# Kernel tuning notes

Measured on AMD Instinct MI355X. Metric: run time of the kernel, lower is better.

## Reference

```python
import jax, jax.numpy as jnp
import numpy as np

B, S, L, H, C = 16, 2048, 256, 768, 512

def setup_inputs() -> dict:
    key = jax.random.key(0)
    ks = jax.random.split(key, 9)
    sc = 1.0 / np.sqrt(H)
    return {
        "input_hidden_states": jax.random.normal(ks[0], (B, S, H), jnp.float32),
        "label_hidden_states": jax.random.normal(ks[1], (L, H), jnp.float32),
        "Wi": jax.random.normal(ks[2], (C, H), jnp.float32) * sc,
        "bi": jnp.zeros((C,), jnp.float32),
        "Wl": jax.random.normal(ks[3], (C, H), jnp.float32) * sc,
        "bl": jnp.zeros((C,), jnp.float32),
        "Wia": jax.random.normal(ks[4], (C, H), jnp.float32) * sc,
        "bia": jnp.zeros((C,), jnp.float32),
        "Wla": jax.random.normal(ks[5], (C, H), jnp.float32) * sc,
        "bla": jnp.zeros((C,), jnp.float32),
        "context": jax.random.uniform(ks[6], (C,), jnp.float32),
        "Wp": jax.random.normal(ks[7], (H, C), jnp.float32) * (1.0 / np.sqrt(C)),
    }

def reference(input_hidden_states, label_hidden_states, Wi, bi, Wl, bl,
              Wia, bia, Wla, bla, context, Wp):
    # Dropout is identity in eval mode.
    x = input_hidden_states            # [B,S,H]
    lab = label_hidden_states          # [L,H] (original repeats over batch; math is identical)
    input_trans = jax.nn.sigmoid(jnp.einsum('bsh,ch->bsc', x, Wi) + bi)      # [B,S,C]
    label_trans = jax.nn.sigmoid(lab @ Wl.T + bl)                            # [L,C]
    input_attn = jax.nn.sigmoid(jnp.einsum('bsh,ch->bsc', x, Wia) + bia)    # [B,S,C]
    label_attn = jax.nn.sigmoid(lab @ Wla.T + bla)                          # [L,C]
    # attn logits: (context * input_attn) @ label_attn^T  -> [B,S,L]
    logits = jnp.einsum('bsc,lc->bsl', input_attn * context, label_attn)
    attn = jax.nn.softmax(logits, axis=-1)                                   # [B,S,L]
    # trilinear reduction: sum_{s,l} input_trans[b,s,c] * attn[b,s,l] * label_trans[l,c]
    weighted = jnp.einsum('bsl,lc->bsc', attn, label_trans)                  # [B,S,C]
    fusion = jnp.sum(input_trans * weighted, axis=1)                         # [B,C]
    return fusion @ Wp.T                                                     # [B,H]
```

## Files before the change

kernel.cpp:

```cpp
#include <hip/hip_runtime.h>

#define H_DIM 768
#define C_DIM 512
#define L_DIM 256
#define S_DIM 2048
#define B_DIM 16

#define IA_STRIDE 520
#define ATTN_STRIDE 264
#define XP_STRIDE 776

typedef __attribute__((ext_vector_type(8))) short short8;
typedef __attribute__((ext_vector_type(4))) float f32x4;
typedef __attribute__((ext_vector_type(2))) __fp16 half2v;

#define MFMA_F16(a, b, c) __builtin_amdgcn_mfma_f32_16x16x32_f16((a), (b), (c), 0, 0, 0)

__device__ __forceinline__ unsigned short f2h(float f) {
    _Float16 h = (_Float16)f;
    return __builtin_bit_cast(unsigned short, h);
}
__device__ __forceinline__ float h2f(unsigned short u) {
    _Float16 h = __builtin_bit_cast(_Float16, u);
    return (float)h;
}
__device__ __forceinline__ float sigmoid_f(float x) { return 1.0f / (1.0f + __expf(-x)); }

__device__ __forceinline__ short8 cvt8(const float* p) {
    const float4* q = (const float4*)(const void*)p;
    float4 u = q[0], v = q[1];
    half2v h0 = __builtin_amdgcn_cvt_pkrtz(u.x, u.y);
    half2v h1 = __builtin_amdgcn_cvt_pkrtz(u.z, u.w);
    half2v h2 = __builtin_amdgcn_cvt_pkrtz(v.x, v.y);
    half2v h3 = __builtin_amdgcn_cvt_pkrtz(v.z, v.w);
    int4 pk = { __builtin_bit_cast(int, h0), __builtin_bit_cast(int, h1),
                __builtin_bit_cast(int, h2), __builtin_bit_cast(int, h3) };
    return __builtin_bit_cast(short8, pk);
}


__global__ __launch_bounds__(256) void prep_w(
    const float* __restrict__ Wi, const float* __restrict__ Wia,
    const float* __restrict__ Wl, const float* __restrict__ Wla,
    unsigned short* __restrict__ Wi_f, unsigned short* __restrict__ Wia_f,
    unsigned short* __restrict__ Wl_f, unsigned short* __restrict__ Wla_f)
{
    const int tid = blockIdx.x * 256 + threadIdx.x;
    const int m   = tid / 49152;
    const int idx = tid - m * 49152;
    const int ct   = idx / 1536;
    const int rem  = idx - ct * 1536;
    const int kt   = rem >> 6;
    const int lane = rem & 63;
    const int row  = ct * 16 + (lane & 15);
    const int kcol = kt * 32 + (lane >> 4) * 8;
    const float* src = (m == 0 ? Wi : (m == 1 ? Wia : (m == 2 ? Wl : Wla)));
    unsigned short* dst = (m == 0 ? Wi_f : (m == 1 ? Wia_f : (m == 2 ? Wl_f : Wla_f)));
    short8 v = cvt8(src + (size_t)row * H_DIM + kcol);
    const int frag = ((ct >> 3) * 24 + kt) * 8 + (ct & 7);
    *(short8*)(void*)(dst + ((size_t)frag * 64 + lane) * 8) = v;
}

__global__ __launch_bounds__(256) void prep_x(
    const float* __restrict__ x, unsigned short* __restrict__ x_f)
{
    __shared__ unsigned short tile[16 * XP_STRIDE];
    const int t  = threadIdx.x;
    const int mt = blockIdx.x;
    const float4* src = (const float4*)(const void*)(x + (size_t)mt * 16 * H_DIM);
#pragma unroll
    for (int i = 0; i < 12; ++i) {
        const int id  = i * 256 + t;
        const int row = id / 192;
        const int c4  = id - row * 192;
        float4 v = src[id];
        half2v h0 = __builtin_amdgcn_cvt_pkrtz(v.x, v.y);
        half2v h1 = __builtin_amdgcn_cvt_pkrtz(v.z, v.w);
        uint2 pk = { __builtin_bit_cast(unsigned int, h0),
                     __builtin_bit_cast(unsigned int, h1) };
        *(uint2*)(void*)(tile + row * XP_STRIDE + c4 * 4) = pk;
    }
    __syncthreads();
    const int lane = t & 63;
    const int wave = t >> 6;
#pragma unroll
    for (int q = 0; q < 6; ++q) {
        const int kt = wave * 6 + q;
        short8 v = *(const short8*)(const void*)(
            tile + (lane & 15) * XP_STRIDE + kt * 32 + (lane >> 4) * 8);
        *(short8*)(void*)(x_f + ((size_t)(mt * 24 + kt) * 64 + lane) * 8) = v;
    }
}

__global__ __launch_bounds__(256) void label_mfma(
    const float* __restrict__ lab,
    const unsigned short* __restrict__ Wl_f,  const float* __restrict__ bl,
    const unsigned short* __restrict__ Wla_f, const float* __restrict__ bla,
    const float* __restrict__ ctx,
    unsigned short* __restrict__ la_f,
    unsigned short* __restrict__ lt_f)
{
    const int tid  = threadIdx.x;
    const int wave = tid >> 6;
    const int lane = tid & 63;
    const int quad = lane >> 4;
    const int c16  = lane & 15;
    const int ct2  = blockIdx.x & 7;
    const int mh   = blockIdx.x >> 3;
    const int ct   = ct2 * 4 + wave;
    const int n0   = ct * 16;
    const int l0   = mh * 32;

    const f32x4 z4 = {0.f, 0.f, 0.f, 0.f};
    f32x4 a1[2], a2[2];
#pragma unroll
    for (int mt = 0; mt < 2; ++mt) { a1[mt] = z4; a2[mt] = z4; }

    const float* lb = lab + (size_t)(l0 + c16) * H_DIM + quad * 8;
    const short8* wl8  = (const short8*)(const void*)Wl_f  + ((size_t)(ct >> 3) * 24 * 8 + (ct & 7)) * 64 + lane;
    const short8* wla8 = (const short8*)(const void*)Wla_f + ((size_t)(ct >> 3) * 24 * 8 + (ct & 7)) * 64 + lane;
    for (int kt = 0; kt < 24; ++kt) {
        short8 b1 = wl8[kt * 8 * 64];
        short8 b2 = wla8[kt * 8 * 64];
#pragma unroll
        for (int mt = 0; mt < 2; ++mt) {
            short8 a = cvt8(lb + mt * 16 * H_DIM + kt * 32);
            a1[mt] = MFMA_F16(a, b1, a1[mt]);
            a2[mt] = MFMA_F16(a, b2, a2[mt]);
        }
    }
    const int c = n0 + c16;
    const float blv = bl[c], blav = bla[c], cv = ctx[c];
#pragma unroll
    for (int mt = 0; mt < 2; ++mt)
#pragma unroll
        for (int r = 0; r < 4; ++r) {
            const int l = l0 + mt * 16 + quad * 4 + r;
            const float ltv = sigmoid_f(a1[mt][r] + blv);
            const float lav = sigmoid_f(a2[mt][r] + blav) * cv;
            {
                const int ctc = c >> 4, ktl = l >> 5;
                const int frag = ((ctc >> 3) * 8 + ktl) * 8 + (ctc & 7);
                const int ln = (c & 15) | (((l >> 3) & 3) << 4);
                lt_f[((size_t)frag * 64 + ln) * 8 + (l & 7)] = f2h(ltv);
            }
            {
                const int lt = l >> 4, ktc = c >> 5;
                const int frag = ((lt >> 2) * 16 + ktc) * 4 + (lt & 3);
                const int ln = (l & 15) | (((c >> 3) & 3) << 4);
                la_f[((size_t)frag * 64 + ln) * 8 + (c & 7)] = f2h(lav);
            }
        }
}

template<bool XF>
__global__ __launch_bounds__(512, 4) void fused_main(
    const unsigned short* __restrict__ x_f,
    const float* __restrict__ x,
    const float* __restrict__ bi,
    const float* __restrict__ bia,
    const unsigned short* __restrict__ Wi_f,
    const unsigned short* __restrict__ Wia_f,
    const unsigned short* __restrict__ lt_f,
    const unsigned short* __restrict__ la_f,
    float* __restrict__ fusion)
{
    __shared__ unsigned short lds_buf[64 * IA_STRIDE];
    __shared__ float rowscratch[8 * 64];
    __shared__ float inv_lds[64];

    const int tid  = threadIdx.x;
    const int wave = tid >> 6;
    const int lane = tid & 63;
    const int quad = lane >> 4;
    const int c16  = lane & 15;

    const int row0 = blockIdx.x * 64;
    const int b    = row0 >> 11;

    const f32x4 z4 = {0.f, 0.f, 0.f, 0.f};
    const int n0 = wave * 64;

    const float*  xb  = x + (size_t)(row0 + c16) * H_DIM + quad * 8;
    const short8* xf8 = (const short8*)(const void*)x_f + (size_t)blockIdx.x * 96 * 64 + lane;
    const size_t wofs = ((size_t)(wave >> 1) * 192 + (size_t)(wave & 1) * 4) * 64 + lane;

    {
        f32x4 acc[4][4];
#pragma unroll
        for (int m = 0; m < 4; ++m)
#pragma unroll
            for (int nt = 0; nt < 4; ++nt) acc[m][nt] = z4;
        const short8* wa8 = (const short8*)(const void*)Wia_f + wofs;
        for (int kt = 0; kt < 24; ++kt) {
            short8 a0, a1, a2, a3;
            if constexpr (XF) {
                a0 = xf8[kt * 64];        a1 = xf8[(24 + kt) * 64];
                a2 = xf8[(48 + kt) * 64]; a3 = xf8[(72 + kt) * 64];
            } else {
                a0 = cvt8(xb + kt * 32);                a1 = cvt8(xb + 16 * H_DIM + kt * 32);
                a2 = cvt8(xb + 32 * H_DIM + kt * 32);   a3 = cvt8(xb + 48 * H_DIM + kt * 32);
            }
#pragma unroll
            for (int nt = 0; nt < 4; ++nt) {
                short8 bw = wa8[(kt * 8 + nt) * 64];
                acc[0][nt] = MFMA_F16(a0, bw, acc[0][nt]);
                acc[1][nt] = MFMA_F16(a1, bw, acc[1][nt]);
                acc[2][nt] = MFMA_F16(a2, bw, acc[2][nt]);
                acc[3][nt] = MFMA_F16(a3, bw, acc[3][nt]);
            }
        }
#pragma unroll
        for (int nt = 0; nt < 4; ++nt) {
            const int col = n0 + nt * 16 + c16;
            const float bv = bia[col];
#pragma unroll
            for (int m = 0; m < 4; ++m)
#pragma unroll
                for (int r = 0; r < 4; ++r) {
                    const int row = m * 16 + quad * 4 + r;
                    lds_buf[row * IA_STRIDE + col] = f2h(sigmoid_f(acc[m][nt][r] + bv));
                }
        }
    }
    __syncthreads();

    const int n0l = wave * 32;
    f32x4 accl[4][2];
#pragma unroll
    for (int m = 0; m < 4; ++m)
#pragma unroll
        for (int j = 0; j < 2; ++j) accl[m][j] = z4;
    {
        const unsigned short* ab = lds_buf + c16 * IA_STRIDE + quad * 8;
        const short8* la8 = (const short8*)(const void*)la_f
                          + ((size_t)(wave >> 1) * 64 + (size_t)(wave & 1) * 2) * 64 + lane;
        for (int kt = 0; kt < 16; ++kt) {
            const int kk = kt * 32;
            short8 a0 = *(const short8*)(const void*)(ab + kk);
            short8 a1 = *(const short8*)(const void*)(ab + 16 * IA_STRIDE + kk);
            short8 a2 = *(const short8*)(const void*)(ab + 32 * IA_STRIDE + kk);
            short8 a3 = *(const short8*)(const void*)(ab + 48 * IA_STRIDE + kk);
#pragma unroll
            for (int j = 0; j < 2; ++j) {
                short8 bfr = la8[(kt * 4 + j) * 64];
                accl[0][j] = MFMA_F16(a0, bfr, accl[0][j]);
                accl[1][j] = MFMA_F16(a1, bfr, accl[1][j]);
                accl[2][j] = MFMA_F16(a2, bfr, accl[2][j]);
                accl[3][j] = MFMA_F16(a3, bfr, accl[3][j]);
            }
        }
    }
    __syncthreads();

    float rmax[4][4];
#pragma unroll
    for (int m = 0; m < 4; ++m)
#pragma unroll
        for (int r = 0; r < 4; ++r) {
            float mx = fmaxf(accl[m][0][r], accl[m][1][r]);
#pragma unroll
            for (int off = 1; off < 16; off <<= 1) mx = fmaxf(mx, __shfl_xor(mx, off, 64));
            rmax[m][r] = mx;
        }
    if (c16 == 0) {
#pragma unroll
        for (int m = 0; m < 4; ++m)
#pragma unroll
            for (int r = 0; r < 4; ++r)
                rowscratch[wave * 64 + m * 16 + quad * 4 + r] = rmax[m][r];
    }
    __syncthreads();
    float rsum[4][4];
#pragma unroll
    for (int m = 0; m < 4; ++m)
#pragma unroll
        for (int r = 0; r < 4; ++r) {
            const int row = m * 16 + quad * 4 + r;
            float gm = rowscratch[row];
#pragma unroll
            for (int w = 1; w < 8; ++w) gm = fmaxf(gm, rowscratch[w * 64 + row]);
            float s = 0.f;
#pragma unroll
            for (int j = 0; j < 2; ++j) {
                float e = __expf(accl[m][j][r] - gm);
                accl[m][j][r] = e;
                s += e;
            }
#pragma unroll
            for (int off = 1; off < 16; off <<= 1) s += __shfl_xor(s, off, 64);
            rsum[m][r] = s;
        }
    __syncthreads();
    if (c16 == 0) {
#pragma unroll
        for (int m = 0; m < 4; ++m)
#pragma unroll
            for (int r = 0; r < 4; ++r)
                rowscratch[wave * 64 + m * 16 + quad * 4 + r] = rsum[m][r];
    }
    __syncthreads();
#pragma unroll
    for (int m = 0; m < 4; ++m)
#pragma unroll
        for (int r = 0; r < 4; ++r) {
            const int row = m * 16 + quad * 4 + r;
            float st = 0.f;
#pragma unroll
            for (int w = 0; w < 8; ++w) st += rowscratch[w * 64 + row];
            if (wave == 0 && c16 == 0) inv_lds[row] = 1.0f / st;
#pragma unroll
            for (int j = 0; j < 2; ++j)
                lds_buf[row * ATTN_STRIDE + n0l + j * 16 + c16] = f2h(accl[m][j][r]);
        }
    __syncthreads();

    f32x4 accw[4][4];
#pragma unroll
    for (int m = 0; m < 4; ++m)
#pragma unroll
        for (int nt = 0; nt < 4; ++nt) accw[m][nt] = z4;
    {
        const unsigned short* ab = lds_buf + c16 * ATTN_STRIDE + quad * 8;
        const short8* lt8 = (const short8*)(const void*)lt_f
                          + ((size_t)(wave >> 1) * 64 + (size_t)(wave & 1) * 4) * 64 + lane;
        for (int kt = 0; kt < 8; ++kt) {
            const int kk = kt * 32;
            short8 a0 = *(const short8*)(const void*)(ab + kk);
            short8 a1 = *(const short8*)(const void*)(ab + 16 * ATTN_STRIDE + kk);
            short8 a2 = *(const short8*)(const void*)(ab + 32 * ATTN_STRIDE + kk);
            short8 a3 = *(const short8*)(const void*)(ab + 48 * ATTN_STRIDE + kk);
#pragma unroll
            for (int nt = 0; nt < 4; ++nt) {
                short8 bfr = lt8[(kt * 8 + nt) * 64];
                accw[0][nt] = MFMA_F16(a0, bfr, accw[0][nt]);
                accw[1][nt] = MFMA_F16(a1, bfr, accw[1][nt]);
                accw[2][nt] = MFMA_F16(a2, bfr, accw[2][nt]);
                accw[3][nt] = MFMA_F16(a3, bfr, accw[3][nt]);
            }
        }
    }
    __syncthreads();

    {
        float invr[4][4];
#pragma unroll
        for (int m = 0; m < 4; ++m)
#pragma unroll
            for (int r = 0; r < 4; ++r) invr[m][r] = inv_lds[m * 16 + quad * 4 + r];
#pragma unroll
        for (int nt = 0; nt < 4; ++nt) {
            const int col = n0 + nt * 16 + c16;
#pragma unroll
            for (int m = 0; m < 4; ++m)
#pragma unroll
                for (int r = 0; r < 4; ++r) {
                    const int row = m * 16 + quad * 4 + r;
                    lds_buf[row * IA_STRIDE + col] = f2h(accw[m][nt][r] * invr[m][r]);
                }
        }
    }

    {
        f32x4 acc[4][4];
#pragma unroll
        for (int m = 0; m < 4; ++m)
#pragma unroll
            for (int nt = 0; nt < 4; ++nt) acc[m][nt] = z4;
        const short8* wi8 = (const short8*)(const void*)Wi_f + wofs;
        for (int kt = 0; kt < 24; ++kt) {
            short8 a0, a1, a2, a3;
            if constexpr (XF) {
                a0 = xf8[kt * 64];        a1 = xf8[(24 + kt) * 64];
                a2 = xf8[(48 + kt) * 64]; a3 = xf8[(72 + kt) * 64];
            } else {
                a0 = cvt8(xb + kt * 32);                a1 = cvt8(xb + 16 * H_DIM + kt * 32);
                a2 = cvt8(xb + 32 * H_DIM + kt * 32);   a3 = cvt8(xb + 48 * H_DIM + kt * 32);
            }
#pragma unroll
            for (int nt = 0; nt < 4; ++nt) {
                short8 bw = wi8[(kt * 8 + nt) * 64];
                acc[0][nt] = MFMA_F16(a0, bw, acc[0][nt]);
                acc[1][nt] = MFMA_F16(a1, bw, acc[1][nt]);
                acc[2][nt] = MFMA_F16(a2, bw, acc[2][nt]);
                acc[3][nt] = MFMA_F16(a3, bw, acc[3][nt]);
            }
        }
#pragma unroll
        for (int nt = 0; nt < 4; ++nt) {
            const int col = n0 + nt * 16 + c16;
            const float bv = bi[col];
            float s = 0.f;
#pragma unroll
            for (int m = 0; m < 4; ++m)
#pragma unroll
                for (int r = 0; r < 4; ++r) {
                    const int row = m * 16 + quad * 4 + r;
                    s += h2f(lds_buf[row * IA_STRIDE + col]) * sigmoid_f(acc[m][nt][r] + bv);
                }
            s += __shfl_xor(s, 16, 64);
            s += __shfl_xor(s, 32, 64);
            if (lane < 16) atomicAdd(&fusion[b * C_DIM + col], s);
        }
    }
}

__global__ __launch_bounds__(256) void out_kernel(
    const float* __restrict__ fusion,
    const float* __restrict__ Wp,
    float* __restrict__ out)
{
    const int idx = blockIdx.x * 256 + threadIdx.x;
    const int R   = idx >> 3;
    const int sub = idx & 7;
    const int bb  = R / H_DIM;
    const int h   = R - bb * H_DIM;
    const float* wp = Wp + (size_t)h * C_DIM;
    const float* f  = fusion + bb * C_DIM;
    float s = 0.f;
#pragma unroll
    for (int j = 0; j < 16; ++j) {
        const int c = j * 32 + sub * 4;
        float4 wv = *(const float4*)(const void*)(wp + c);
        float4 fv = *(const float4*)(const void*)(f + c);
        s += fv.x * wv.x + fv.y * wv.y + fv.z * wv.z + fv.w * wv.w;
    }
    s += __shfl_xor(s, 1, 64);
    s += __shfl_xor(s, 2, 64);
    s += __shfl_xor(s, 4, 64);
    if (sub == 0) out[R] = s;
}

extern "C" void kernel_launch(void* const* d_in, const int* in_sizes, int n_in,
                              void* d_out, int out_size, void* d_ws, size_t ws_size,
                              hipStream_t stream)
{
    const float* x    = (const float*)d_in[0];
    const float* lab  = (const float*)d_in[1];
    const float* Wi   = (const float*)d_in[2];
    const float* bi   = (const float*)d_in[3];
    const float* Wl   = (const float*)d_in[4];
    const float* bl   = (const float*)d_in[5];
    const float* Wia  = (const float*)d_in[6];
    const float* bia  = (const float*)d_in[7];
    const float* Wla  = (const float*)d_in[8];
    const float* bla  = (const float*)d_in[9];
    const float* ctx  = (const float*)d_in[10];
    const float* Wp   = (const float*)d_in[11];

    char* ws = (char*)d_ws;
    unsigned short* Wi_f  = (unsigned short*)(ws);
    unsigned short* Wia_f = (unsigned short*)(ws + 786432);
    unsigned short* Wl_f  = (unsigned short*)(ws + 1572864);
    unsigned short* Wla_f = (unsigned short*)(ws + 2359296);
    unsigned short* la_f  = (unsigned short*)(ws + 3145728);
    unsigned short* lt_f  = (unsigned short*)(ws + 3407872);
    float* fusion         = (float*)(ws + 3670016);
    unsigned short* x_f   = (unsigned short*)(ws + 3702784);
    const size_t NEED_XF  = 3702784 + (size_t)32768 * 768 * 2;

    (void)hipMemsetAsync(fusion, 0, B_DIM * C_DIM * sizeof(float), stream);
    prep_w<<<768, 256, 0, stream>>>(Wi, Wia, Wl, Wla, Wi_f, Wia_f, Wl_f, Wla_f);
    label_mfma<<<64, 256, 0, stream>>>(lab, Wl_f, bl, Wla_f, bla, ctx, la_f, lt_f);
    if (ws_size >= NEED_XF) {
        prep_x<<<2048, 256, 0, stream>>>(x, x_f);
        fused_main<true><<<(B_DIM * S_DIM) / 64, 512, 0, stream>>>(
            x_f, x, bi, bia, Wi_f, Wia_f, lt_f, la_f, fusion);
    } else {
        fused_main<false><<<(B_DIM * S_DIM) / 64, 512, 0, stream>>>(
            nullptr, x, bi, bia, Wi_f, Wia_f, lt_f, la_f, fusion);
    }
    out_kernel<<<384, 256, 0, stream>>>(fusion, Wp, (float*)d_out);
}
```

Measured before the change: 293.8 us.

## Use 1024-thread blocks, fuse Wi/Wia GEMMs, keep input_trans in registers, merge prep kernels

The main kernel now runs 16 waves per block, each owning 32 output columns. The Wi and Wia projections are computed in a single pass over x, so the x fragments are read once instead of twice. input_trans is kept as packed fp16 in registers rather than recomputed after the attention stage, and the softmax is restructured so the sum and the normalization need fewer barriers. The x and W prep kernels are merged into one launch, and label_mfma converts Wl/Wla on the fly, which removes one kernel launch. The risks are higher register pressure from holding both accumulator sets at 1024 threads per block, and less latency hiding from fewer resident blocks.

Measured after the change: 310.6 us. 1.06x slower.

```diff
diff --git a/kernel.cpp b/kernel.cpp
--- a/kernel.cpp
+++ b/kernel.cpp
@@ -38,64 +38,79 @@
     return __builtin_bit_cast(short8, pk);
 }
 
-
-__global__ __launch_bounds__(256) void prep_w(
+__device__ __forceinline__ float max16f(const float* p) {
+    const float4* q = (const float4*)(const void*)p;
+    float4 a = q[0], b = q[1], c = q[2], d = q[3];
+    float m0 = fmaxf(fmaxf(a.x, a.y), fmaxf(a.z, a.w));
+    float m1 = fmaxf(fmaxf(b.x, b.y), fmaxf(b.z, b.w));
+    float m2 = fmaxf(fmaxf(c.x, c.y), fmaxf(c.z, c.w));
+    float m3 = fmaxf(fmaxf(d.x, d.y), fmaxf(d.z, d.w));
+    return fmaxf(fmaxf(m0, m1), fmaxf(m2, m3));
+}
+__device__ __forceinline__ float sum16f(const float* p) {
+    const float4* q = (const float4*)(const void*)p;
+    float4 a = q[0], b = q[1], c = q[2], d = q[3];
+    return ((a.x + a.y) + (a.z + a.w)) + ((b.x + b.y) + (b.z + b.w))
+         + ((c.x + c.y) + (c.z + c.w)) + ((d.x + d.y) + (d.z + d.w));
+}
+
+
+__global__ __launch_bounds__(256) void prep_xw(
+    const float* __restrict__ x,
     const float* __restrict__ Wi, const float* __restrict__ Wia,
-    const float* __restrict__ Wl, const float* __restrict__ Wla,
+    unsigned short* __restrict__ x_f,
     unsigned short* __restrict__ Wi_f, unsigned short* __restrict__ Wia_f,
-    unsigned short* __restrict__ Wl_f, unsigned short* __restrict__ Wla_f)
-{
-    const int tid = blockIdx.x * 256 + threadIdx.x;
-    const int m   = tid / 49152;
-    const int idx = tid - m * 49152;
-    const int ct   = idx / 1536;
-    const int rem  = idx - ct * 1536;
-    const int kt   = rem >> 6;
-    const int lane = rem & 63;
-    const int row  = ct * 16 + (lane & 15);
-    const int kcol = kt * 32 + (lane >> 4) * 8;
-    const float* src = (m == 0 ? Wi : (m == 1 ? Wia : (m == 2 ? Wl : Wla)));
-    unsigned short* dst = (m == 0 ? Wi_f : (m == 1 ? Wia_f : (m == 2 ? Wl_f : Wla_f)));
-    short8 v = cvt8(src + (size_t)row * H_DIM + kcol);
-    const int frag = ((ct >> 3) * 24 + kt) * 8 + (ct & 7);
-    *(short8*)(void*)(dst + ((size_t)frag * 64 + lane) * 8) = v;
-}
-
-__global__ __launch_bounds__(256) void prep_x(
-    const float* __restrict__ x, unsigned short* __restrict__ x_f)
+    int xblocks)
 {
     __shared__ unsigned short tile[16 * XP_STRIDE];
-    const int t  = threadIdx.x;
-    const int mt = blockIdx.x;
-    const float4* src = (const float4*)(const void*)(x + (size_t)mt * 16 * H_DIM);
-#pragma unroll
-    for (int i = 0; i < 12; ++i) {
-        const int id  = i * 256 + t;
-        const int row = id / 192;
-        const int c4  = id - row * 192;
-        float4 v = src[id];
-        half2v h0 = __builtin_amdgcn_cvt_pkrtz(v.x, v.y);
-        half2v h1 = __builtin_amdgcn_cvt_pkrtz(v.z, v.w);
-        uint2 pk = { __builtin_bit_cast(unsigned int, h0),
-                     __builtin_bit_cast(unsigned int, h1) };
-        *(uint2*)(void*)(tile + row * XP_STRIDE + c4 * 4) = pk;
-    }
-    __syncthreads();
-    const int lane = t & 63;
-    const int wave = t >> 6;
-#pragma unroll
-    for (int q = 0; q < 6; ++q) {
-        const int kt = wave * 6 + q;
-        short8 v = *(const short8*)(const void*)(
-            tile + (lane & 15) * XP_STRIDE + kt * 32 + (lane >> 4) * 8);
-        *(short8*)(void*)(x_f + ((size_t)(mt * 24 + kt) * 64 + lane) * 8) = v;
+    const int t = threadIdx.x;
+    if ((int)blockIdx.x < xblocks) {
+        const int mt = blockIdx.x;
+        const float4* src = (const float4*)(const void*)(x + (size_t)mt * 16 * H_DIM);
+#pragma unroll
+        for (int i = 0; i < 12; ++i) {
+            const int id  = i * 256 + t;
+            const int row = id / 192;
+            const int c4  = id - row * 192;
+            float4 v = src[id];
+            half2v h0 = __builtin_amdgcn_cvt_pkrtz(v.x, v.y);
+            half2v h1 = __builtin_amdgcn_cvt_pkrtz(v.z, v.w);
+            uint2 pk = { __builtin_bit_cast(unsigned int, h0),
+                         __builtin_bit_cast(unsigned int, h1) };
+            *(uint2*)(void*)(tile + row * XP_STRIDE + c4 * 4) = pk;
+        }
+        __syncthreads();
+        const int lane = t & 63;
+        const int wave = t >> 6;
+#pragma unroll
+        for (int q = 0; q < 6; ++q) {
+            const int kt = wave * 6 + q;
+            short8 v = *(const short8*)(const void*)(
+                tile + (lane & 15) * XP_STRIDE + kt * 32 + (lane >> 4) * 8);
+            *(short8*)(void*)(x_f + ((size_t)(mt * 24 + kt) * 64 + lane) * 8) = v;
+        }
+    } else {
+        const int tid = (blockIdx.x - xblocks) * 256 + t;
+        const int m   = tid / 49152;
+        const int idx = tid - m * 49152;
+        const int ct   = idx / 1536;
+        const int rem  = idx - ct * 1536;
+        const int kt   = rem >> 6;
+        const int lane = rem & 63;
+        const int row  = ct * 16 + (lane & 15);
+        const int kcol = kt * 32 + (lane >> 4) * 8;
+        const float* src = (m == 0 ? Wi : Wia);
+        unsigned short* dst = (m == 0 ? Wi_f : Wia_f);
+        short8 v = cvt8(src + (size_t)row * H_DIM + kcol);
+        const int frag = ((ct >> 3) * 24 + kt) * 8 + (ct & 7);
+        *(short8*)(void*)(dst + ((size_t)frag * 64 + lane) * 8) = v;
     }
 }
 
 __global__ __launch_bounds__(256) void label_mfma(
     const float* __restrict__ lab,
-    const unsigned short* __restrict__ Wl_f,  const float* __restrict__ bl,
-    const unsigned short* __restrict__ Wla_f, const float* __restrict__ bla,
+    const float* __restrict__ Wl,  const float* __restrict__ bl,
+    const float* __restrict__ Wla, const float* __restrict__ bla,
     const float* __restrict__ ctx,
     unsigned short* __restrict__ la_f,
     unsigned short* __restrict__ lt_f)
@@ -116,12 +131,12 @@
 #pragma unroll
     for (int mt = 0; mt < 2; ++mt) { a1[mt] = z4; a2[mt] = z4; }
 
-    const float* lb = lab + (size_t)(l0 + c16) * H_DIM + quad * 8;
-    const short8* wl8  = (const short8*)(const void*)Wl_f  + ((size_t)(ct >> 3) * 24 * 8 + (ct & 7)) * 64 + lane;
-    const short8* wla8 = (const short8*)(const void*)Wla_f + ((size_t)(ct >> 3) * 24 * 8 + (ct & 7)) * 64 + lane;
+    const float* lb   = lab + (size_t)(l0 + c16) * H_DIM + quad * 8;
+    const float* wlp  = Wl  + (size_t)(n0 + c16) * H_DIM + quad * 8;
+    const float* wlap = Wla + (size_t)(n0 + c16) * H_DIM + quad * 8;
     for (int kt = 0; kt < 24; ++kt) {
-        short8 b1 = wl8[kt * 8 * 64];
-        short8 b2 = wla8[kt * 8 * 64];
+        short8 b1 = cvt8(wlp + kt * 32);
+        short8 b2 = cvt8(wlap + kt * 32);
 #pragma unroll
         for (int mt = 0; mt < 2; ++mt) {
             short8 a = cvt8(lb + mt * 16 * H_DIM + kt * 32);
@@ -154,7 +169,7 @@
 }
 
 template<bool XF>
-__global__ __launch_bounds__(512, 4) void fused_main(
+__global__ __launch_bounds__(1024) void fused_main(
     const unsigned short* __restrict__ x_f,
     const float* __restrict__ x,
     const float* __restrict__ bi,
@@ -166,8 +181,8 @@
     float* __restrict__ fusion)
 {
     __shared__ unsigned short lds_buf[64 * IA_STRIDE];
-    __shared__ float rowscratch[8 * 64];
-    __shared__ float inv_lds[64];
+    __shared__ float scratchA[64 * 16];
+    __shared__ float scratchB[64 * 16];
 
     const int tid  = threadIdx.x;
     const int wave = tid >> 6;
@@ -179,19 +194,23 @@
     const int b    = row0 >> 11;
 
     const f32x4 z4 = {0.f, 0.f, 0.f, 0.f};
-    const int n0 = wave * 64;
+    const int n0  = wave * 32;
+    const int ct0 = wave * 2;
 
     const float*  xb  = x + (size_t)(row0 + c16) * H_DIM + quad * 8;
     const short8* xf8 = (const short8*)(const void*)x_f + (size_t)blockIdx.x * 96 * 64 + lane;
-    const size_t wofs = ((size_t)(wave >> 1) * 192 + (size_t)(wave & 1) * 4) * 64 + lane;
+    const size_t wofs = ((size_t)(ct0 >> 3) * 192 + (ct0 & 7)) * 64 + lane;
+    const short8* wa8 = (const short8*)(const void*)Wia_f + wofs;
+    const short8* wi8 = (const short8*)(const void*)Wi_f  + wofs;
+
+    unsigned int it_h[4][2][2];
 
     {
-        f32x4 acc[4][4];
+        f32x4 aa[4][2], at[4][2];
 #pragma unroll
         for (int m = 0; m < 4; ++m)
 #pragma unroll
-            for (int nt = 0; nt < 4; ++nt) acc[m][nt] = z4;
-        const short8* wa8 = (const short8*)(const void*)Wia_f + wofs;
+            for (int nt = 0; nt < 2; ++nt) { aa[m][nt] = z4; at[m][nt] = z4; }
         for (int kt = 0; kt < 24; ++kt) {
             short8 a0, a1, a2, a3;
             if constexpr (XF) {
@@ -201,207 +220,152 @@
                 a0 = cvt8(xb + kt * 32);                a1 = cvt8(xb + 16 * H_DIM + kt * 32);
                 a2 = cvt8(xb + 32 * H_DIM + kt * 32);   a3 = cvt8(xb + 48 * H_DIM + kt * 32);
             }
-#pragma unroll
-            for (int nt = 0; nt < 4; ++nt) {
-                short8 bw = wa8[(kt * 8 + nt) * 64];
-                acc[0][nt] = MFMA_F16(a0, bw, acc[0][nt]);
-                acc[1][nt] = MFMA_F16(a1, bw, acc[1][nt]);
-                acc[2][nt] = MFMA_F16(a2, bw, acc[2][nt]);
-                acc[3][nt] = MFMA_F16(a3, bw, acc[3][nt]);
-            }
-        }
-#pragma unroll
-        for (int nt = 0; nt < 4; ++nt) {
+            const int ko = kt * 512;
+            {
+                short8 ba = wa8[ko], bt = wi8[ko];
+                aa[0][0] = MFMA_F16(a0, ba, aa[0][0]);
+                aa[1][0] = MFMA_F16(a1, ba, aa[1][0]);
+                aa[2][0] = MFMA_F16(a2, ba, aa[2][0]);
+                aa[3][0] = MFMA_F16(a3, ba, aa[3][0]);
+                at[0][0] = MFMA_F16(a0, bt, at[0][0]);
+                at[1][0] = MFMA_F16(a1, bt, at[1][0]);
+                at[2][0] = MFMA_F16(a2, bt, at[2][0]);
+                at[3][0] = MFMA_F16(a3, bt, at[3][0]);
+            }
+            {
+                short8 ba = wa8[ko + 64], bt = wi8[ko + 64];
+                aa[0][1] = MFMA_F16(a0, ba, aa[0][1]);
+                aa[1][1] = MFMA_F16(a1, ba, aa[1][1]);
+                aa[2][1] = MFMA_F16(a2, ba, aa[2][1]);
+                aa[3][1] = MFMA_F16(a3, ba, aa[3][1]);
+                at[0][1] = MFMA_F16(a0, bt, at[0][1]);
+                at[1][1] = MFMA_F16(a1, bt, at[1][1]);
+                at[2][1] = MFMA_F16(a2, bt, at[2][1]);
+                at[3][1] = MFMA_F16(a3, bt, at[3][1]);
+            }
+        }
+#pragma unroll
+        for (int nt = 0; nt < 2; ++nt) {
             const int col = n0 + nt * 16 + c16;
-            const float bv = bia[col];
-#pragma unroll
-            for (int m = 0; m < 4; ++m)
+            const float bav = bia[col], biv = bi[col];
+#pragma unroll
+            for (int m = 0; m < 4; ++m) {
 #pragma unroll
                 for (int r = 0; r < 4; ++r) {
                     const int row = m * 16 + quad * 4 + r;
-                    lds_buf[row * IA_STRIDE + col] = f2h(sigmoid_f(acc[m][nt][r] + bv));
+                    lds_buf[row * IA_STRIDE + col] = f2h(sigmoid_f(aa[m][nt][r] + bav));
                 }
+                const float t0 = sigmoid_f(at[m][nt][0] + biv);
+                const float t1 = sigmoid_f(at[m][nt][1] + biv);
+                const float t2 = sigmoid_f(at[m][nt][2] + biv);
+                const float t3 = sigmoid_f(at[m][nt][3] + biv);
+                it_h[m][nt][0] = __builtin_bit_cast(unsigned int, __builtin_amdgcn_cvt_pkrtz(t0, t1));
+                it_h[m][nt][1] = __builtin_bit_cast(unsigned int, __builtin_amdgcn_cvt_pkrtz(t2, t3));
+            }
         }
     }
     __syncthreads();
 
-    const int n0l = wave * 32;
-    f32x4 accl[4][2];
-#pragma unroll
-    for (int m = 0; m < 4; ++m)
-#pragma unroll
-        for (int j = 0; j < 2; ++j) accl[m][j] = z4;
+    f32x4 accl[4];
+#pragma unroll
+    for (int m = 0; m < 4; ++m) accl[m] = z4;
     {
         const unsigned short* ab = lds_buf + c16 * IA_STRIDE + quad * 8;
         const short8* la8 = (const short8*)(const void*)la_f
-                          + ((size_t)(wave >> 1) * 64 + (size_t)(wave & 1) * 2) * 64 + lane;
+                          + ((size_t)(wave >> 2) * 64 + (wave & 3)) * 64 + lane;
         for (int kt = 0; kt < 16; ++kt) {
             const int kk = kt * 32;
             short8 a0 = *(const short8*)(const void*)(ab + kk);
             short8 a1 = *(const short8*)(const void*)(ab + 16 * IA_STRIDE + kk);
             short8 a2 = *(const short8*)(const void*)(ab + 32 * IA_STRIDE + kk);
             short8 a3 = *(const short8*)(const void*)(ab + 48 * IA_STRIDE + kk);
-#pragma unroll
-            for (int j = 0; j < 2; ++j) {
-                short8 bfr = la8[(kt * 4 + j) * 64];
-                accl[0][j] = MFMA_F16(a0, bfr, accl[0][j]);
-                accl[1][j] = MFMA_F16(a1, bfr, accl[1][j]);
-                accl[2][j] = MFMA_F16(a2, bfr, accl[2][j]);
-                accl[3][j] = MFMA_F16(a3, bfr, accl[3][j]);
-            }
+            short8 bfr = la8[kt * 256];
+            accl[0] = MFMA_F16(a0, bfr, accl[0]);
+            accl[1] = MFMA_F16(a1, bfr, accl[1]);
+            accl[2] = MFMA_F16(a2, bfr, accl[2]);
+            accl[3] = MFMA_F16(a3, bfr, accl[3]);
         }
     }
     __syncthreads();
 
-    float rmax[4][4];
 #pragma unroll
     for (int m = 0; m < 4; ++m)
 #pragma unroll
         for (int r = 0; r < 4; ++r) {
-            float mx = fmaxf(accl[m][0][r], accl[m][1][r]);
+            float mx = accl[m][r];
 #pragma unroll
             for (int off = 1; off < 16; off <<= 1) mx = fmaxf(mx, __shfl_xor(mx, off, 64));
-            rmax[m][r] = mx;
-        }
-    if (c16 == 0) {
-#pragma unroll
-        for (int m = 0; m < 4; ++m)
-#pragma unroll
-            for (int r = 0; r < 4; ++r)
-                rowscratch[wave * 64 + m * 16 + quad * 4 + r] = rmax[m][r];
-    }
+            if (c16 == 0) scratchA[(m * 16 + quad * 4 + r) * 16 + wave] = mx;
+        }
     __syncthreads();
-    float rsum[4][4];
 #pragma unroll
     for (int m = 0; m < 4; ++m)
 #pragma unroll
         for (int r = 0; r < 4; ++r) {
             const int row = m * 16 + quad * 4 + r;
-            float gm = rowscratch[row];
-#pragma unroll
-            for (int w = 1; w < 8; ++w) gm = fmaxf(gm, rowscratch[w * 64 + row]);
-            float s = 0.f;
-#pragma unroll
-            for (int j = 0; j < 2; ++j) {
-                float e = __expf(accl[m][j][r] - gm);
-                accl[m][j][r] = e;
-                s += e;
-            }
-#pragma unroll
-            for (int off = 1; off < 16; off <<= 1) s += __shfl_xor(s, off, 64);
-            rsum[m][r] = s;
+            const float gm = max16f(&scratchA[row * 16]);
+            float e = __expf(accl[m][r] - gm);
+            lds_buf[row * ATTN_STRIDE + wave * 16 + c16] = f2h(e);
+#pragma unroll
+            for (int off = 1; off < 16; off <<= 1) e += __shfl_xor(e, off, 64);
+            if (c16 == 0) scratchB[row * 16 + wave] = e;
         }
     __syncthreads();
-    if (c16 == 0) {
-#pragma unroll
-        for (int m = 0; m < 4; ++m)
-#pragma unroll
-            for (int r = 0; r < 4; ++r)
-                rowscratch[wave * 64 + m * 16 + quad * 4 + r] = rsum[m][r];
-    }
-    __syncthreads();
+    float invr[4][4];
 #pragma unroll
     for (int m = 0; m < 4; ++m)
 #pragma unroll
         for (int r = 0; r < 4; ++r) {
             const int row = m * 16 + quad * 4 + r;
-            float st = 0.f;
-#pragma unroll
-            for (int w = 0; w < 8; ++w) st += rowscratch[w * 64 + row];
-            if (wave == 0 && c16 == 0) inv_lds[row] = 1.0f / st;
-#pragma unroll
-            for (int j = 0; j < 2; ++j)
-                lds_buf[row * ATTN_STRIDE + n0l + j * 16 + c16] = f2h(accl[m][j][r]);
-        }
-    __syncthreads();
-
-    f32x4 accw[4][4];
+            invr[m][r] = 1.0f / sum16f(&scratchB[row * 16]);
+        }
+
+    f32x4 accw[4][2];
 #pragma unroll
     for (int m = 0; m < 4; ++m)
 #pragma unroll
-        for (int nt = 0; nt < 4; ++nt) accw[m][nt] = z4;
+        for (int nt = 0; nt < 2; ++nt) accw[m][nt] = z4;
     {
         const unsigned short* ab = lds_buf + c16 * ATTN_STRIDE + quad * 8;
         const short8* lt8 = (const short8*)(const void*)lt_f
-                          + ((size_t)(wave >> 1) * 64 + (size_t)(wave & 1) * 4) * 64 + lane;
+                          + ((size_t)(ct0 >> 3) * 64 + (ct0 & 7)) * 64 + lane;
         for (int kt = 0; kt < 8; ++kt) {
             const int kk = kt * 32;
             short8 a0 = *(const short8*)(const void*)(ab + kk);
             short8 a1 = *(const short8*)(const void*)(ab + 16 * ATTN_STRIDE + kk);
             short8 a2 = *(const short8*)(const void*)(ab + 32 * ATTN_STRIDE + kk);
             short8 a3 = *(const short8*)(const void*)(ab + 48 * ATTN_STRIDE + kk);
-#pragma unroll
-            for (int nt = 0; nt < 4; ++nt) {
-                short8 bfr = lt8[(kt * 8 + nt) * 64];
-                accw[0][nt] = MFMA_F16(a0, bfr, accw[0][nt]);
-                accw[1][nt] = MFMA_F16(a1, bfr, accw[1][nt]);
-                accw[2][nt] = MFMA_F16(a2, bfr, accw[2][nt]);
-                accw[3][nt] = MFMA_F16(a3, bfr, accw[3][nt]);
-            }
-        }
-    }
-    __syncthreads();
-
-    {
-        float invr[4][4];
-#pragma unroll
-        for (int m = 0; m < 4; ++m)
-#pragma unroll
-            for (int r = 0; r < 4; ++r) invr[m][r] = inv_lds[m * 16 + quad * 4 + r];
-#pragma unroll
-        for (int nt = 0; nt < 4; ++nt) {
-            const int col = n0 + nt * 16 + c16;
-#pragma unroll
-            for (int m = 0; m < 4; ++m)
-#pragma unroll
-                for (int r = 0; r < 4; ++r) {
-                    const int row = m * 16 + quad * 4 + r;
-                    lds_buf[row * IA_STRIDE + col] = f2h(accw[m][nt][r] * invr[m][r]);
-                }
-        }
-    }
-
-    {
-        f32x4 acc[4][4];
-#pragma unroll
-        for (int m = 0; m < 4; ++m)
-#pragma unroll
-            for (int nt = 0; nt < 4; ++nt) acc[m][nt] = z4;
-        const short8* wi8 = (const short8*)(const void*)Wi_f + wofs;
-        for (int kt = 0; kt < 24; ++kt) {
-            short8 a0, a1, a2, a3;
-            if constexpr (XF) {
-                a0 = xf8[kt * 64];        a1 = xf8[(24 + kt) * 64];
-                a2 = xf8[(48 + kt) * 64]; a3 = xf8[(72 + kt) * 64];
-            } else {
-                a0 = cvt8(xb + kt * 32);                a1 = cvt8(xb + 16 * H_DIM + kt * 32);
-                a2 = cvt8(xb + 32 * H_DIM + kt * 32);   a3 = cvt8(xb + 48 * H_DIM + kt * 32);
-            }
-#pragma unroll
-            for (int nt = 0; nt < 4; ++nt) {
-                short8 bw = wi8[(kt * 8 + nt) * 64];
-                acc[0][nt] = MFMA_F16(a0, bw, acc[0][nt]);
-                acc[1][nt] = MFMA_F16(a1, bw, acc[1][nt]);
-                acc[2][nt] = MFMA_F16(a2, bw, acc[2][nt]);
-                acc[3][nt] = MFMA_F16(a3, bw, acc[3][nt]);
-            }
-        }
-#pragma unroll
-        for (int nt = 0; nt < 4; ++nt) {
-            const int col = n0 + nt * 16 + c16;
-            const float bv = bi[col];
-            float s = 0.f;
-#pragma unroll
-            for (int m = 0; m < 4; ++m)
-#pragma unroll
-                for (int r = 0; r < 4; ++r) {
-                    const int row = m * 16 + quad * 4 + r;
-                    s += h2f(lds_buf[row * IA_STRIDE + col]) * sigmoid_f(acc[m][nt][r] + bv);
-                }
-            s += __shfl_xor(s, 16, 64);
-            s += __shfl_xor(s, 32, 64);
-            if (lane < 16) atomicAdd(&fusion[b * C_DIM + col], s);
-        }
+            short8 b0 = lt8[kt * 512], b1 = lt8[kt * 512 + 64];
+            accw[0][0] = MFMA_F16(a0, b0, accw[0][0]);
+            accw[1][0] = MFMA_F16(a1, b0, accw[1][0]);
+            accw[2][0] = MFMA_F16(a2, b0, accw[2][0]);
+            accw[3][0] = MFMA_F16(a3, b0, accw[3][0]);
+            accw[0][1] = MFMA_F16(a0, b1, accw[0][1]);
+            accw[1][1] = MFMA_F16(a1, b1, accw[1][1]);
+            accw[2][1] = MFMA_F16(a2, b1, accw[2][1]);
+            accw[3][1] = MFMA_F16(a3, b1, accw[3][1]);
+        }
+    }
+
+#pragma unroll
+    for (int nt = 0; nt < 2; ++nt) {
+        const int col = n0 + nt * 16 + c16;
+        float s = 0.f;
+#pragma unroll
+        for (int m = 0; m < 4; ++m) {
+            const unsigned int u0 = it_h[m][nt][0], u1 = it_h[m][nt][1];
+            const float t0 = h2f((unsigned short)(u0 & 0xffff));
+            const float t1 = h2f((unsigned short)(u0 >> 16));
+            const float t2 = h2f((unsigned short)(u1 & 0xffff));
+            const float t3 = h2f((unsigned short)(u1 >> 16));
+            s += accw[m][nt][0] * invr[m][0] * t0;
+            s += accw[m][nt][1] * invr[m][1] * t1;
+            s += accw[m][nt][2] * invr[m][2] * t2;
+            s += accw[m][nt][3] * invr[m][3] * t3;
+        }
+        s += __shfl_xor(s, 16, 64);
+        s += __shfl_xor(s, 32, 64);
+        if (lane < 16) atomicAdd(&fusion[b * C_DIM + col], s);
     }
 }
 
@@ -451,8 +415,6 @@
     char* ws = (char*)d_ws;
     unsigned short* Wi_f  = (unsigned short*)(ws);
     unsigned short* Wia_f = (unsigned short*)(ws + 786432);
-    unsigned short* Wl_f  = (unsigned short*)(ws + 1572864);
-    unsigned short* Wla_f = (unsigned short*)(ws + 2359296);
     unsigned short* la_f  = (unsigned short*)(ws + 3145728);
     unsigned short* lt_f  = (unsigned short*)(ws + 3407872);
     float* fusion         = (float*)(ws + 3670016);
@@ -460,14 +422,14 @@
     const size_t NEED_XF  = 3702784 + (size_t)32768 * 768 * 2;
 
     (void)hipMemsetAsync(fusion, 0, B_DIM * C_DIM * sizeof(float), stream);
-    prep_w<<<768, 256, 0, stream>>>(Wi, Wia, Wl, Wla, Wi_f, Wia_f, Wl_f, Wla_f);
-    label_mfma<<<64, 256, 0, stream>>>(lab, Wl_f, bl, Wla_f, bla, ctx, la_f, lt_f);
+    label_mfma<<<64, 256, 0, stream>>>(lab, Wl, bl, Wla, bla, ctx, la_f, lt_f);
     if (ws_size >= NEED_XF) {
-        prep_x<<<2048, 256, 0, stream>>>(x, x_f);
-        fused_main<true><<<(B_DIM * S_DIM) / 64, 512, 0, stream>>>(
+        prep_xw<<<2048 + 384, 256, 0, stream>>>(x, Wi, Wia, x_f, Wi_f, Wia_f, 2048);
+        fused_main<true><<<(B_DIM * S_DIM) / 64, 1024, 0, stream>>>(
             x_f, x, bi, bia, Wi_f, Wia_f, lt_f, la_f, fusion);
     } else {
-        fused_main<false><<<(B_DIM * S_DIM) / 64, 512, 0, stream>>>(
+        prep_xw<<<384, 256, 0, stream>>>(x, Wi, Wia, x_f, Wi_f, Wia_f, 0);
+        fused_main<false><<<(B_DIM * S_DIM) / 64, 1024, 0, stream>>>(
             nullptr, x, bi, bia, Wi_f, Wia_f, lt_f, la_f, fusion);
     }
     out_kernel<<<384, 256, 0, stream>>>(fusion, Wp, (float*)d_out);
```
